# Kernel optimization log

Hardware: AMD Instinct MI355X
Metric: run time of the kernel (lower is better)

## Reference

```python
import jax, jax.numpy as jnp
import numpy as np
from jax import lax

N, CIN, COUT, T, V, S = 64, 64, 64, 256, 25, 3
REL = CIN // 8  # 8, per __init__ branch for in_channels=64


def setup_inputs() -> dict:
    key = jax.random.key(0)
    ks = jax.random.split(key, 22)
    rn = lambda i, shape, s=0.05: jax.random.normal(ks[i], shape, jnp.float32) * s
    return dict(
        x=jax.random.normal(ks[0], (N, CIN, T, V), jnp.float32),
        A=rn(1, (S, V, V), 0.2),                 # adaptive PA parameter
        alpha=jnp.asarray(0.1, jnp.float32),     # unit_gcn alpha (scalar)
        w1=rn(2, (S, REL, CIN)), b1=rn(3, (S, REL)),
        w2=rn(4, (S, REL, CIN)), b2=rn(5, (S, REL)),
        w3=rn(6, (S, COUT, CIN)), b3=rn(7, (S, COUT)),
        w4=rn(8, (S, COUT, REL)), b4=rn(9, (S, COUT)),
        pm_w1=rn(10, (S, REL, 2 * REL)), pm_b1=rn(11, (S, REL)),
        pm_w2=rn(12, (S, REL, REL)), pm_b2=rn(13, (S, REL)),
        dw_w=rn(14, (S, REL, 1, 3, 3)),          # depthwise 3x3, groups=REL
        proj_w=rn(15, (S, COUT, REL)),           # aux_proj, no bias
        beta=rn(16, (S,), 0.01), gamma=rn(17, (S,), 0.01),
        bn_w=jnp.ones((COUT,), jnp.float32), bn_b=jnp.zeros((COUT,), jnp.float32),
    )


def _sorgc(x, Ai, alpha, w1, b1, w2, b2, w3, b3, w4, b4,
           pw1, pb1, pw2, pb2, dww, pjw, beta, gamma):
    # x: (N, C, T, V)
    xm = x.mean(axis=2)                                            # (N,C,V) -- 1x1 conv is linear, so conv then mean == mean then conv
    x1 = jnp.einsum('ncv,rc->nrv', xm, w1) + b1[:, None]           # (N,R,V)
    x2 = jnp.einsum('ncv,rc->nrv', xm, w2) + b2[:, None]
    x3 = jnp.einsum('nctv,oc->notv', x, w3) + b3[:, None, None]    # (N,O,T,V)
    q1 = jnp.tanh(x1[:, :, :, None] - x2[:, :, None, :])           # (N,R,V,V)
    psi = jnp.broadcast_to(x2[:, :, :, None], q1.shape)
    phi = jnp.broadcast_to(x2[:, :, None, :], q1.shape)
    pair = jnp.concatenate([psi, phi], axis=1)                     # (N,2R,V,V)
    h = jax.nn.relu(jnp.einsum('npuv,rp->nruv', pair, pw1) + pb1[:, None, None])
    q2 = jnp.einsum('npuv,rp->nruv', h, pw2) + pb2[:, None, None]
    q_all = q1 + gamma * q2
    R = (jnp.einsum('nruv,or->nouv', q_all, w4) + b4[:, None, None]) * alpha + Ai[None, None]
    # aux branch: depthwise 3x3 conv -> avgpool3x3 (count_include_pad) -> tanh -> 1x1 proj
    Ra = lax.conv_general_dilated(q1, dww, (1, 1), [(1, 1), (1, 1)],
                                  dimension_numbers=('NCHW', 'OIHW', 'NCHW'),
                                  feature_group_count=q1.shape[1])
    Ra = lax.reduce_window(Ra, 0.0, lax.add, (1, 1, 3, 3), (1, 1, 1, 1),
                           [(0, 0), (0, 0), (1, 1), (1, 1)]) / 9.0
    Ra = jnp.tanh(Ra)
    Ra = jnp.einsum('nruv,or->nouv', Ra, pjw)                      # (N,O,V,V)
    R = R + beta * Ra
    return jnp.einsum('ncuv,nctv->nctu', R, x3)                    # (N,O,T,V)


def reference(x, A, alpha, w1, b1, w2, b2, w3, b3, w4, b4,
              pm_w1, pm_b1, pm_w2, pm_b2, dw_w, proj_w, beta, gamma, bn_w, bn_b):
    y = None
    for i in range(S):
        z = _sorgc(x, A[i], alpha, w1[i], b1[i], w2[i], b2[i], w3[i], b3[i],
                   w4[i], b4[i], pm_w1[i], pm_b1[i], pm_w2[i], pm_b2[i],
                   dw_w[i], proj_w[i], beta[i], gamma[i])
        y = z if y is None else y + z
    # BatchNorm2d (training-mode batch statistics), eps=1e-5
    mu = y.mean(axis=(0, 2, 3), keepdims=True)
    var = y.var(axis=(0, 2, 3), keepdims=True)
    y = (y - mu) * lax.rsqrt(var + 1e-5) * bn_w[None, :, None, None] + bn_b[None, :, None, None]
    y = y + x  # residual (in_channels == out_channels -> identity down)
    return jax.nn.relu(y)
```

## Files before the change

kernel.cpp:

```cpp
#include <hip/hip_runtime.h>


#define WS_R_BYTE   409600
#define WS_BN_BYTE  17711104

typedef __attribute__((ext_vector_type(8))) short bf16x8;
typedef __attribute__((ext_vector_type(4))) float f32x4;

static __device__ __forceinline__ unsigned short f2bf(float f) {
    unsigned int u = __float_as_uint(f);
    u += 0x7fff + ((u >> 16) & 1);
    return (unsigned short)(u >> 16);
}
static __device__ __forceinline__ float bf2f(unsigned short s) {
    return __uint_as_float(((unsigned int)s) << 16);
}

__global__ __launch_bounds__(256) void k_xm(const float* __restrict__ x,
                                            float* __restrict__ ws) {
    int idx = blockIdx.x * 256 + threadIdx.x;
    int n = idx / 1600;
    int cv = idx % 1600;
    int c = cv / 25, v = cv % 25;
    const float* xp = x + (n * 64 + c) * 6400 + v;
    float s = 0.f;
    #pragma unroll 8
    for (int t = 0; t < 256; t++) s += xp[t * 25];
    ws[idx] = s * (1.f / 256.f);
}

__global__ __launch_bounds__(512) void k_small(
    const float* __restrict__ ws, unsigned short* __restrict__ Rg,
    const float* __restrict__ A, const float* __restrict__ alphap,
    const float* __restrict__ w1, const float* __restrict__ b1,
    const float* __restrict__ w2, const float* __restrict__ b2,
    const float* __restrict__ w4, const float* __restrict__ b4,
    const float* __restrict__ pw1, const float* __restrict__ pb1,
    const float* __restrict__ pw2, const float* __restrict__ pb2,
    const float* __restrict__ dww, const float* __restrict__ pjw,
    const float* __restrict__ beta, const float* __restrict__ gamma) {
    __shared__ float sm[15000];
    const int tid = threadIdx.x;
    const int s = blockIdx.x >> 6;
    const int n = blockIdx.x & 63;
    const float alpha = alphap[0];
    const float gam = gamma[s], bet = beta[s];

    for (int i = tid; i < 1600; i += 512) sm[5000 + i] = ws[n * 1600 + i];
    __syncthreads();

    for (int i = tid; i < 400; i += 512) {
        int half = i / 200, j = i % 200;
        int r = j / 25, k = j % 25;
        const float* w = (half ? w2 : w1) + (s * 8 + r) * 64;
        float acc = (half ? b2 : b1)[s * 8 + r];
        for (int c = 0; c < 64; c++) acc += w[c] * sm[5000 + c * 25 + k];
        sm[6600 + i] = acc;
    }
    __syncthreads();

    for (int i = tid; i < 5400; i += 512) {
        if (i < 5000) {
            int r = i / 625, uv = i % 625, u = uv / 25, v = uv % 25;
            sm[i] = tanhf(sm[6600 + r * 25 + u] - sm[6800 + r * 25 + v]);
        } else {
            int i2 = i - 5000;
            int half = i2 / 200, j = i2 % 200;
            int r = j / 25, k = j % 25;
            float acc = 0.f;
            for (int p = 0; p < 8; p++)
                acc += pw1[(s * 8 + r) * 16 + half * 8 + p] * sm[6800 + p * 25 + k];
            sm[7000 + i2] = acc;
        }
    }
    __syncthreads();

    for (int i = tid; i < 5000; i += 512) {
        int r = i / 625, uv = i % 625, u = uv / 25, v = uv % 25;
        float t = sm[7000 + r * 25 + u] + sm[7200 + r * 25 + v] + pb1[s * 8 + r];
        sm[10000 + i] = t > 0.f ? t : 0.f;
    }
    __syncthreads();

    for (int i = tid; i < 5000; i += 512) {
        int r = i / 625, uv = i % 625;
        float q2 = pb2[s * 8 + r];
        for (int p = 0; p < 8; p++)
            q2 += pw2[(s * 8 + r) * 8 + p] * sm[10000 + p * 625 + uv];
        sm[5000 + i] = sm[i] + gam * q2;
    }
    __syncthreads();

    for (int i = tid; i < 5000; i += 512) {
        int r = i / 625, uv = i % 625, u = uv / 25, v = uv % 25;
        float acc = 0.f;
        for (int di = 0; di < 3; di++) {
            int uu = u + di - 1;
            if (uu < 0 || uu > 24) continue;
            for (int dj = 0; dj < 3; dj++) {
                int vv = v + dj - 1;
                if (vv < 0 || vv > 24) continue;
                acc += sm[r * 625 + uu * 25 + vv] * dww[(s * 8 + r) * 9 + di * 3 + dj];
            }
        }
        sm[10000 + i] = acc;
    }
    __syncthreads();

    for (int i = tid; i < 5000; i += 512) {
        int r = i / 625, uv = i % 625, u = uv / 25, v = uv % 25;
        float acc = 0.f;
        for (int di = 0; di < 3; di++) {
            int uu = u + di - 1;
            if (uu < 0 || uu > 24) continue;
            for (int dj = 0; dj < 3; dj++) {
                int vv = v + dj - 1;
                if (vv < 0 || vv > 24) continue;
                acc += sm[10000 + r * 625 + uu * 25 + vv];
            }
        }
        sm[i] = tanhf(acc * (1.f / 9.f));
    }
    __syncthreads();

    unsigned short* Rb = Rg + (unsigned)((s * 64 + n) * 64) * 704;
    for (int i = tid; i < 40000; i += 512) {
        int o = i / 625, vu = i % 625, vv = vu / 25, uu = vu % 25;
        int quv = uu * 25 + vv;
        float mn = b4[s * 64 + o], aux = 0.f;
        for (int r = 0; r < 8; r++) {
            mn  += w4[(s * 64 + o) * 8 + r] * sm[5000 + r * 625 + quv];
            aux += pjw[(s * 64 + o) * 8 + r] * sm[r * 625 + quv];
        }
        Rb[o * 704 + vv * 28 + uu] = f2bf(mn * alpha + A[s * 625 + quv] + bet * aux);
    }
    for (int i = tid; i < 64 * 25 * 3; i += 512) {
        int o = i / 75, rem = i % 75, vv = rem / 3, uu = 25 + rem % 3;
        Rb[o * 704 + vv * 28 + uu] = 0;
    }
}

__global__ __launch_bounds__(256, 2) void k_main(
    const float* __restrict__ x, const float* __restrict__ w3,
    const float* __restrict__ b3, const unsigned short* __restrict__ Rg,
    float* __restrict__ out) {
    __shared__ __align__(16) unsigned short xb[400 * 64];
    __shared__ __align__(16) unsigned short Rs[64 * 84];
    const int tid  = threadIdx.x;
    const int n    = blockIdx.x >> 4;
    const int t0   = (blockIdx.x & 15) * 16;
    const int lane = tid & 63;
    const int w    = tid >> 6;
    const int ln15 = lane & 15;
    const int q    = lane >> 4;
    const int og   = w * 16 + ln15;

    {
        const float* xbase = x + n * 409600 + t0 * 25;
        #pragma unroll 5
        for (int k = 0; k < 25; k++) {
            int i  = tid + k * 256;
            int tv = i % 400;
            int cq = i / 400;
            const float* p = xbase + cq * 4 * 6400 + tv;
            ushort4 h;
            h.x = f2bf(p[0]); h.y = f2bf(p[6400]); h.z = f2bf(p[12800]); h.w = f2bf(p[19200]);
            int addr = tv * 64 + (((cq >> 1) ^ (tv & 7)) << 3) + ((cq & 1) << 2);
            *(ushort4*)&xb[addr] = h;
        }
    }

    float yacc[26][4];
    #pragma unroll
    for (int u = 0; u < 26; u++)
        #pragma unroll
        for (int r = 0; r < 4; r++) yacc[u][r] = 0.f;

    for (int s = 0; s < 3; s++) {
        bf16x8 bfr[2];
        {
            const float* wp = w3 + (s * 64 + og) * 64;
            #pragma unroll
            for (int ks = 0; ks < 2; ks++)
                #pragma unroll
                for (int j = 0; j < 8; j++)
                    bfr[ks][j] = (short)f2bf(wp[ks * 32 + q * 8 + j]);
        }
        const float bias = b3[s * 64 + og];
        const unsigned short* Rsrc = Rg + (unsigned)((s * 64 + n) * 64) * 704;

        for (int vg = 0; vg < 9; vg++) {
            const int nv = (vg < 8) ? 3 : 1;
            __syncthreads();
            {
                const int cpo = 7 * nv;
                const int nchunks = 64 * cpo;
                for (int i = tid; i < nchunks; i += 256) {
                    int o = i / cpo, ch = i % cpo;
                    *(ushort4*)&Rs[o * 84 + ch * 4] =
                        *(const ushort4*)&Rsrc[o * 704 + vg * 84 + ch * 4];
                }
            }
            __syncthreads();

            f32x4 c[3];
            #pragma unroll
            for (int iv = 0; iv < 3; iv++) {
                if (iv >= nv) break;
                const int v   = vg * 3 + iv;
                const int row = ln15 * 25 + v;
                const int sw  = row & 7;
                bf16x8 a0 = *(const bf16x8*)&xb[row * 64 + ((q ^ sw) << 3)];
                bf16x8 a1 = *(const bf16x8*)&xb[row * 64 + (((4 + q) ^ sw) << 3)];
                f32x4 cc; cc[0] = bias; cc[1] = bias; cc[2] = bias; cc[3] = bias;
                cc = __builtin_amdgcn_mfma_f32_16x16x32_bf16(a0, bfr[0], cc, 0, 0, 0);
                cc = __builtin_amdgcn_mfma_f32_16x16x32_bf16(a1, bfr[1], cc, 0, 0, 0);
                c[iv] = cc;
            }
            #pragma unroll
            for (int iv = 0; iv < 3; iv++) {
                if (iv >= nv) break;
                const unsigned short* rr = &Rs[og * 84 + iv * 28];
                f32x4 cc = c[iv];
                #pragma unroll
                for (int ug = 0; ug < 6; ug++) {
                    ushort4 r4 = *(const ushort4*)(rr + ug * 4);
                    float f0 = bf2f(r4.x), f1 = bf2f(r4.y);
                    float f2 = bf2f(r4.z), f3 = bf2f(r4.w);
                    #pragma unroll
                    for (int r = 0; r < 4; r++) {
                        yacc[ug * 4 + 0][r] += f0 * cc[r];
                        yacc[ug * 4 + 1][r] += f1 * cc[r];
                        yacc[ug * 4 + 2][r] += f2 * cc[r];
                        yacc[ug * 4 + 3][r] += f3 * cc[r];
                    }
                }
                float f24 = bf2f(rr[24]);
                #pragma unroll
                for (int r = 0; r < 4; r++) yacc[24][r] += f24 * cc[r];
            }
        }
    }

    float* op = out + (n * 64 + og) * 6400 + t0 * 25;
    #pragma unroll
    for (int r = 0; r < 4; r++) {
        float* opr = op + (q * 4 + r) * 25;
        #pragma unroll
        for (int u = 0; u < 25; u++) opr[u] = yacc[u][r];
    }
}

__global__ __launch_bounds__(256) void k_bnstat(const float* __restrict__ y,
                                                float* __restrict__ bnacc) {
    const int tid = threadIdx.x;
    const int o = blockIdx.x >> 3;
    const int ch = blockIdx.x & 7;
    float s = 0.f, s2 = 0.f;
    for (int nn = 0; nn < 8; nn++) {
        const int n = ch * 8 + nn;
        const float4* p = (const float4*)(y + (n * 64 + o) * 6400);
        for (int i = tid; i < 1600; i += 256) {
            float4 v = p[i];
            s  += v.x + v.y + v.z + v.w;
            s2 += v.x * v.x + v.y * v.y + v.z * v.z + v.w * v.w;
        }
    }
    for (int off = 32; off > 0; off >>= 1) {
        s  += __shfl_down(s, off);
        s2 += __shfl_down(s2, off);
    }
    __shared__ float ls[4], ls2[4];
    int wid = tid >> 6;
    if ((tid & 63) == 0) { ls[wid] = s; ls2[wid] = s2; }
    __syncthreads();
    if (tid == 0) {
        atomicAdd(bnacc + o,      ls[0] + ls[1] + ls[2] + ls[3]);
        atomicAdd(bnacc + 64 + o, ls2[0] + ls2[1] + ls2[2] + ls2[3]);
    }
}

__global__ __launch_bounds__(256) void k_final(
    float* __restrict__ out, const float* __restrict__ x,
    const float* __restrict__ bnacc,
    const float* __restrict__ bnw, const float* __restrict__ bnb) {
    const int idx4 = blockIdx.x * 256 + threadIdx.x;
    const int o = (idx4 / 1600) & 63;
    const float cnt = 1.f / 409600.f;
    float mean = bnacc[o] * cnt;
    float var = bnacc[64 + o] * cnt - mean * mean;
    float inv = rsqrtf(var + 1e-5f);
    float sc = bnw[o] * inv;
    float sh = bnb[o] - mean * sc;
    float4 y = ((const float4*)out)[idx4];
    float4 xv = ((const float4*)x)[idx4];
    y.x = fmaxf(y.x * sc + sh + xv.x, 0.f);
    y.y = fmaxf(y.y * sc + sh + xv.y, 0.f);
    y.z = fmaxf(y.z * sc + sh + xv.z, 0.f);
    y.w = fmaxf(y.w * sc + sh + xv.w, 0.f);
    ((float4*)out)[idx4] = y;
}

extern "C" void kernel_launch(void* const* d_in, const int* in_sizes, int n_in,
                              void* d_out, int out_size, void* d_ws, size_t ws_size,
                              hipStream_t stream) {
    const float* x     = (const float*)d_in[0];
    const float* A     = (const float*)d_in[1];
    const float* alpha = (const float*)d_in[2];
    const float* w1    = (const float*)d_in[3];
    const float* b1    = (const float*)d_in[4];
    const float* w2    = (const float*)d_in[5];
    const float* b2    = (const float*)d_in[6];
    const float* w3    = (const float*)d_in[7];
    const float* b3    = (const float*)d_in[8];
    const float* w4    = (const float*)d_in[9];
    const float* b4    = (const float*)d_in[10];
    const float* pw1   = (const float*)d_in[11];
    const float* pb1   = (const float*)d_in[12];
    const float* pw2   = (const float*)d_in[13];
    const float* pb2   = (const float*)d_in[14];
    const float* dww   = (const float*)d_in[15];
    const float* pjw   = (const float*)d_in[16];
    const float* beta  = (const float*)d_in[17];
    const float* gamma = (const float*)d_in[18];
    const float* bnw   = (const float*)d_in[19];
    const float* bnb   = (const float*)d_in[20];
    float* out = (float*)d_out;
    float* ws  = (float*)d_ws;
    unsigned short* wsR = (unsigned short*)((char*)d_ws + WS_R_BYTE);
    float* wsBN = (float*)((char*)d_ws + WS_BN_BYTE);

    k_xm<<<400, 256, 0, stream>>>(x, ws);
    k_small<<<192, 512, 0, stream>>>(ws, wsR, A, alpha, w1, b1, w2, b2,
                                     w4, b4, pw1, pb1, pw2, pb2, dww, pjw,
                                     beta, gamma);
    hipMemsetAsync(wsBN, 0, 128 * sizeof(float), stream);
    k_main<<<1024, 256, 0, stream>>>(x, w3, b3, wsR, out);
    k_bnstat<<<512, 256, 0, stream>>>(out, wsBN);
    k_final<<<25600, 256, 0, stream>>>(out, x, wsBN, bnw, bnb);
}
```

Baseline: 533.7 us.

## Fuse BN statistics into main kernel, async double-buffer R tiles, coalesce mean

Several changes land together. k_main now folds the BatchNorm sum and sum-of-squares into its epilogue with padded atomics, so the separate k_bnstat pass that re-read the output is gone. R tiles are stored pre-tiled in the order they are consumed and streamed into LDS through global_load_lds in a double buffer, which removes one barrier per tile and overlaps the copies with compute. k_xm is rewritten to stage each (n,c) plane in LDS with coalesced float4 loads, and the block index is swizzled. The BN accumulator now reuses the xm workspace region, which is safe only because k_small has finished reading it, and atomic contention rises with 16 lanes per channel across 1024 blocks.

```diff
diff --git a/kernel.cpp b/kernel.cpp
--- a/kernel.cpp
+++ b/kernel.cpp
@@ -2,10 +2,12 @@
 
 
 #define WS_R_BYTE   409600
-#define WS_BN_BYTE  17711104
 
 typedef __attribute__((ext_vector_type(8))) short bf16x8;
 typedef __attribute__((ext_vector_type(4))) float f32x4;
+
+typedef __attribute__((address_space(1))) unsigned int uint_g;
+typedef __attribute__((address_space(3))) unsigned int uint_l;
 
 static __device__ __forceinline__ unsigned short f2bf(float f) {
     unsigned int u = __float_as_uint(f);
@@ -15,18 +17,33 @@
 static __device__ __forceinline__ float bf2f(unsigned short s) {
     return __uint_as_float(((unsigned int)s) << 16);
 }
+static __device__ __forceinline__ void gload_lds16(const void* g, void* l) {
+    __builtin_amdgcn_global_load_lds((const uint_g*)g, (uint_l*)l, 16, 0, 0);
+}
 
 __global__ __launch_bounds__(256) void k_xm(const float* __restrict__ x,
                                             float* __restrict__ ws) {
-    int idx = blockIdx.x * 256 + threadIdx.x;
-    int n = idx / 1600;
-    int cv = idx % 1600;
-    int c = cv / 25, v = cv % 25;
-    const float* xp = x + (n * 64 + c) * 6400 + v;
-    float s = 0.f;
-    #pragma unroll 8
-    for (int t = 0; t < 256; t++) s += xp[t * 25];
-    ws[idx] = s * (1.f / 256.f);
+    __shared__ float sm[6400];
+    __shared__ float part[200];
+    const int tid = threadIdx.x;
+    const int n = blockIdx.x >> 6, c = blockIdx.x & 63;
+    const float4* p = (const float4*)(x + (unsigned)(n * 64 + c) * 6400u);
+    float4* s4 = (float4*)sm;
+    for (int i = tid; i < 1600; i += 256) s4[i] = p[i];
+    __syncthreads();
+    if (tid < 200) {
+        int v = tid % 25, g = tid / 25;
+        float s = 0.f;
+        for (int tt = 0; tt < 32; tt++) s += sm[(g * 32 + tt) * 25 + v];
+        part[tid] = s;
+    }
+    __syncthreads();
+    if (tid < 25) {
+        float s = 0.f;
+        #pragma unroll
+        for (int g = 0; g < 8; g++) s += part[g * 25 + tid];
+        ws[n * 1600 + c * 25 + tid] = s * (1.f / 256.f);
+    }
 }
 
 __global__ __launch_bounds__(512) void k_small(
@@ -123,37 +140,61 @@
     }
     __syncthreads();
 
-    unsigned short* Rb = Rg + (unsigned)((s * 64 + n) * 64) * 704;
-    for (int i = tid; i < 40000; i += 512) {
-        int o = i / 625, vu = i % 625, vv = vu / 25, uu = vu % 25;
-        int quv = uu * 25 + vv;
-        float mn = b4[s * 64 + o], aux = 0.f;
-        for (int r = 0; r < 8; r++) {
-            mn  += w4[(s * 64 + o) * 8 + r] * sm[5000 + r * 625 + quv];
-            aux += pjw[(s * 64 + o) * 8 + r] * sm[r * 625 + quv];
-        }
-        Rb[o * 704 + vv * 28 + uu] = f2bf(mn * alpha + A[s * 625 + quv] + bet * aux);
-    }
-    for (int i = tid; i < 64 * 25 * 3; i += 512) {
-        int o = i / 75, rem = i % 75, vv = rem / 3, uu = 25 + rem % 3;
-        Rb[o * 704 + vv * 28 + uu] = 0;
+    unsigned short* Rb = Rg + (unsigned)(s * 64 + n) * 44800u;
+    for (int i = tid; i < 44800; i += 512) {
+        int o, vv, uu;
+        if (i < 43008) {
+            int vg = i / 5376, rem = i % 5376;
+            o = rem / 84;
+            int j = rem % 84;
+            vv = vg * 3 + j / 28;
+            uu = j % 28;
+        } else {
+            int rem = i - 43008;
+            o = rem / 28;
+            vv = 24;
+            uu = rem % 28;
+        }
+        unsigned short val = 0;
+        if (uu < 25) {
+            int quv = uu * 25 + vv;
+            float mn = b4[s * 64 + o], aux = 0.f;
+            for (int r = 0; r < 8; r++) {
+                mn  += w4[(s * 64 + o) * 8 + r] * sm[5000 + r * 625 + quv];
+                aux += pjw[(s * 64 + o) * 8 + r] * sm[r * 625 + quv];
+            }
+            val = f2bf(mn * alpha + A[s * 625 + quv] + bet * aux);
+        }
+        Rb[i] = val;
     }
 }
 
 __global__ __launch_bounds__(256, 2) void k_main(
     const float* __restrict__ x, const float* __restrict__ w3,
     const float* __restrict__ b3, const unsigned short* __restrict__ Rg,
-    float* __restrict__ out) {
-    __shared__ __align__(16) unsigned short xb[400 * 64];
-    __shared__ __align__(16) unsigned short Rs[64 * 84];
+    float* __restrict__ out, float* __restrict__ bnacc) {
+    __shared__ __align__(16) unsigned char smem[73728];
+    unsigned short* xb = (unsigned short*)smem;
+    unsigned char* RsBase = smem + 51200;
+
     const int tid  = threadIdx.x;
-    const int n    = blockIdx.x >> 4;
-    const int t0   = (blockIdx.x & 15) * 16;
+    const int blk  = ((int)blockIdx.x & 7) * 128 + ((int)blockIdx.x >> 3);
+    const int n    = blk >> 4;
+    const int t0   = (blk & 15) * 16;
     const int lane = tid & 63;
     const int w    = tid >> 6;
     const int ln15 = lane & 15;
     const int q    = lane >> 4;
     const int og   = w * 16 + ln15;
+
+    const unsigned short* Rn0 = Rg;
+
+    {
+        const char* src = (const char*)Rg + (size_t)((0 * 64 + n) * 44800) * 2;
+        unsigned char* dst = RsBase;
+        for (int j = w; j < 11; j += 4)
+            gload_lds16(src + j * 1024 + (lane << 4), dst + j * 1024);
+    }
 
     {
         const float* xbase = x + n * 409600 + t0 * 25;
@@ -164,18 +205,21 @@
             int cq = i / 400;
             const float* p = xbase + cq * 4 * 6400 + tv;
             ushort4 h;
-            h.x = f2bf(p[0]); h.y = f2bf(p[6400]); h.z = f2bf(p[12800]); h.w = f2bf(p[19200]);
+            h.x = f2bf(p[0]); h.y = f2bf(p[6400]);
+            h.z = f2bf(p[12800]); h.w = f2bf(p[19200]);
             int addr = tv * 64 + (((cq >> 1) ^ (tv & 7)) << 3) + ((cq & 1) << 2);
             *(ushort4*)&xb[addr] = h;
         }
     }
-
-    float yacc[26][4];
+    __syncthreads();
+
+    float yacc[25][4];
     #pragma unroll
-    for (int u = 0; u < 26; u++)
+    for (int u = 0; u < 25; u++)
         #pragma unroll
         for (int r = 0; r < 4; r++) yacc[u][r] = 0.f;
 
+    int buf = 0;
     for (int s = 0; s < 3; s++) {
         bf16x8 bfr[2];
         {
@@ -187,21 +231,23 @@
                     bfr[ks][j] = (short)f2bf(wp[ks * 32 + q * 8 + j]);
         }
         const float bias = b3[s * 64 + og];
-        const unsigned short* Rsrc = Rg + (unsigned)((s * 64 + n) * 64) * 704;
 
         for (int vg = 0; vg < 9; vg++) {
+            {
+                int ns = s, nvg = vg + 1;
+                if (nvg == 9) { ns = s + 1; nvg = 0; }
+                if (ns < 3) {
+                    const char* src = (const char*)Rg +
+                        (size_t)((ns * 64 + n) * 44800 + nvg * 5376) * 2;
+                    unsigned char* dst = RsBase + (buf ^ 1) * 11264;
+                    const int rounds = (nvg < 8) ? 11 : 4;
+                    for (int j = w; j < rounds; j += 4)
+                        gload_lds16(src + j * 1024 + (lane << 4), dst + j * 1024);
+                }
+            }
+
+            const unsigned short* RsB = (const unsigned short*)(RsBase + buf * 11264);
             const int nv = (vg < 8) ? 3 : 1;
-            __syncthreads();
-            {
-                const int cpo = 7 * nv;
-                const int nchunks = 64 * cpo;
-                for (int i = tid; i < nchunks; i += 256) {
-                    int o = i / cpo, ch = i % cpo;
-                    *(ushort4*)&Rs[o * 84 + ch * 4] =
-                        *(const ushort4*)&Rsrc[o * 704 + vg * 84 + ch * 4];
-                }
-            }
-            __syncthreads();
 
             f32x4 c[3];
             #pragma unroll
@@ -220,7 +266,8 @@
             #pragma unroll
             for (int iv = 0; iv < 3; iv++) {
                 if (iv >= nv) break;
-                const unsigned short* rr = &Rs[og * 84 + iv * 28];
+                const unsigned short* rr = (vg < 8) ? &RsB[og * 84 + iv * 28]
+                                                    : &RsB[og * 28];
                 f32x4 cc = c[iv];
                 #pragma unroll
                 for (int ug = 0; ug < 6; ug++) {
@@ -239,44 +286,29 @@
                 #pragma unroll
                 for (int r = 0; r < 4; r++) yacc[24][r] += f24 * cc[r];
             }
+
+            __syncthreads();
+            buf ^= 1;
         }
     }
 
     float* op = out + (n * 64 + og) * 6400 + t0 * 25;
+    float s1 = 0.f, s2 = 0.f;
     #pragma unroll
     for (int r = 0; r < 4; r++) {
         float* opr = op + (q * 4 + r) * 25;
         #pragma unroll
-        for (int u = 0; u < 25; u++) opr[u] = yacc[u][r];
-    }
-}
-
-__global__ __launch_bounds__(256) void k_bnstat(const float* __restrict__ y,
-                                                float* __restrict__ bnacc) {
-    const int tid = threadIdx.x;
-    const int o = blockIdx.x >> 3;
-    const int ch = blockIdx.x & 7;
-    float s = 0.f, s2 = 0.f;
-    for (int nn = 0; nn < 8; nn++) {
-        const int n = ch * 8 + nn;
-        const float4* p = (const float4*)(y + (n * 64 + o) * 6400);
-        for (int i = tid; i < 1600; i += 256) {
-            float4 v = p[i];
-            s  += v.x + v.y + v.z + v.w;
-            s2 += v.x * v.x + v.y * v.y + v.z * v.z + v.w * v.w;
-        }
-    }
-    for (int off = 32; off > 0; off >>= 1) {
-        s  += __shfl_down(s, off);
-        s2 += __shfl_down(s2, off);
-    }
-    __shared__ float ls[4], ls2[4];
-    int wid = tid >> 6;
-    if ((tid & 63) == 0) { ls[wid] = s; ls2[wid] = s2; }
-    __syncthreads();
-    if (tid == 0) {
-        atomicAdd(bnacc + o,      ls[0] + ls[1] + ls[2] + ls[3]);
-        atomicAdd(bnacc + 64 + o, ls2[0] + ls2[1] + ls2[2] + ls2[3]);
+        for (int u = 0; u < 25; u++) {
+            float vv = yacc[u][r];
+            opr[u] = vv;
+            s1 += vv; s2 += vv * vv;
+        }
+    }
+    s1 += __shfl_xor(s1, 16); s1 += __shfl_xor(s1, 32);
+    s2 += __shfl_xor(s2, 16); s2 += __shfl_xor(s2, 32);
+    if (q == 0) {
+        atomicAdd(&bnacc[og * 16], s1);
+        atomicAdd(&bnacc[1024 + og * 16], s2);
     }
 }
 
@@ -287,8 +319,8 @@
     const int idx4 = blockIdx.x * 256 + threadIdx.x;
     const int o = (idx4 / 1600) & 63;
     const float cnt = 1.f / 409600.f;
-    float mean = bnacc[o] * cnt;
-    float var = bnacc[64 + o] * cnt - mean * mean;
+    float mean = bnacc[o * 16] * cnt;
+    float var = bnacc[1024 + o * 16] * cnt - mean * mean;
     float inv = rsqrtf(var + 1e-5f);
     float sc = bnw[o] * inv;
     float sh = bnb[o] - mean * sc;
@@ -328,14 +360,13 @@
     float* out = (float*)d_out;
     float* ws  = (float*)d_ws;
     unsigned short* wsR = (unsigned short*)((char*)d_ws + WS_R_BYTE);
-    float* wsBN = (float*)((char*)d_ws + WS_BN_BYTE);
-
-    k_xm<<<400, 256, 0, stream>>>(x, ws);
+    float* wsBN = ws;
+
+    k_xm<<<4096, 256, 0, stream>>>(x, ws);
     k_small<<<192, 512, 0, stream>>>(ws, wsR, A, alpha, w1, b1, w2, b2,
                                      w4, b4, pw1, pb1, pw2, pb2, dww, pjw,
                                      beta, gamma);
-    hipMemsetAsync(wsBN, 0, 128 * sizeof(float), stream);
-    k_main<<<1024, 256, 0, stream>>>(x, w3, b3, wsR, out);
-    k_bnstat<<<512, 256, 0, stream>>>(out, wsBN);
+    hipMemsetAsync(wsBN, 0, 8192, stream);
+    k_main<<<1024, 256, 0, stream>>>(x, w3, b3, wsR, out, wsBN);
     k_final<<<25600, 256, 0, stream>>>(out, x, wsBN, bnw, bnb);
 }
```

Result: faster. 434.0 us (-18.7%).
